# Optimization experiments

Hardware: AMD Instinct MI355X
Metric: run time of the kernel (lower is better)

The kernel has to match this reference:

```python
import jax, jax.numpy as jnp
import numpy as np

N, E, D, HID, HEADS, G = 20000, 320000, 1280, 64, 4, 256
NEG_SLOPE = 0.2  # PyG GATv2Conv default negative_slope


def setup_inputs() -> dict:
    key = jax.random.key(0)
    ks = jax.random.split(key, 20)

    def w(k, shape, fan_in):
        return (jax.random.normal(k, shape, jnp.float32) / np.float32(np.sqrt(fan_in)))

    return {
        "x": jax.random.normal(ks[0], (N, D), jnp.float32),
        "edge_index": jax.random.randint(ks[1], (2, E), 0, N),
        "batch": jnp.sort(jax.random.randint(ks[2], (N,), 0, G)),
        # GATv2 layer 1: in D, out HID, heads HEADS, concat
        "Wl1": w(ks[3], (D, HEADS * HID), D),
        "bl1": w(ks[4], (HEADS * HID,), D),
        "Wr1": w(ks[5], (D, HEADS * HID), D),
        "br1": w(ks[6], (HEADS * HID,), D),
        "att1": w(ks[7], (HEADS, HID), HID),
        "bias1": jnp.zeros((HEADS * HID,), jnp.float32),
        # GATv2 layer 2: in HEADS*HID, out HID, heads 1, concat
        "Wl2": w(ks[8], (HEADS * HID, HID), HEADS * HID),
        "bl2": w(ks[9], (HID,), HEADS * HID),
        "Wr2": w(ks[10], (HEADS * HID, HID), HEADS * HID),
        "br2": w(ks[11], (HID,), HEADS * HID),
        "att2": w(ks[12], (1, HID), HID),
        "bias2": jnp.zeros((HID,), jnp.float32),
        # MLP head
        "W3": w(ks[13], (HID, HID), HID),
        "b3": w(ks[14], (HID,), HID),
        "W4": w(ks[15], (HID, 1), HID),
        "b4": w(ks[16], (1,), HID),
    }


def _gatv2(x, src, dst, Wl, bl, Wr, br, att, bias, n):
    """PyG GATv2Conv (concat=True, eval mode): e_ij = a^T LeakyReLU(Wl x_j + Wr x_i),
    per-destination softmax, out_i = sum_j alpha_ij * (Wl x_j)."""
    H, C = att.shape
    xl = (x @ Wl + bl).reshape(n, H, C)  # source transform
    xr = (x @ Wr + br).reshape(n, H, C)  # target transform
    e = jax.nn.leaky_relu(xl[src] + xr[dst], NEG_SLOPE)      # [E,H,C]
    logit = jnp.einsum('ehc,hc->eh', e, att)                  # [E,H]
    m = jax.ops.segment_max(logit, dst, num_segments=n)      # stable softmax per dst
    ex = jnp.exp(logit - m[dst])
    denom = jax.ops.segment_sum(ex, dst, num_segments=n)
    alpha = ex / (denom[dst] + 1e-16)                         # [E,H]
    out = jax.ops.segment_sum(xl[src] * alpha[:, :, None], dst, num_segments=n)
    return out.reshape(n, H * C) + bias


def reference(x, edge_index, batch, Wl1, bl1, Wr1, br1, att1, bias1,
              Wl2, bl2, Wr2, br2, att2, bias2, W3, b3, W4, b4):
    # add_self_loops=True (PyG default)
    loops = jnp.arange(N, dtype=edge_index.dtype)
    src = jnp.concatenate([edge_index[0], loops])
    dst = jnp.concatenate([edge_index[1], loops])
    h = jax.nn.relu(_gatv2(x, src, dst, Wl1, bl1, Wr1, br1, att1, bias1, N))
    h = jax.nn.relu(_gatv2(h, src, dst, Wl2, bl2, Wr2, br2, att2, bias2, N))
    g = jax.ops.segment_sum(h, batch, num_segments=G)  # global_add_pool -> [G,HID]
    return jax.nn.relu(g @ W3 + b3) @ W4 + b4          # [G,1]
```

## Files before the change

kernel.cpp:

```cpp
#include <hip/hip_runtime.h>

constexpr int Nn    = 20000;
constexpr int Ee    = 320000;
constexpr int Dd    = 1280;
constexpr int Gg    = 256;
constexpr int ETOT  = Ee + Nn;
#define NEG 0.2f

typedef __attribute__((ext_vector_type(8))) short s8v;
typedef __attribute__((ext_vector_type(8))) unsigned short u16x8;
typedef __attribute__((ext_vector_type(4))) float f4v;

__device__ inline float lrelu(float v){ return v > 0.f ? v : NEG * v; }
__device__ inline float wave_sum(float v){
  #pragma unroll
  for(int o = 32; o; o >>= 1) v += __shfl_xor(v, o, 64);
  return v;
}
__device__ inline unsigned short f2bf(float x){
  unsigned u = __float_as_uint(x);
  return (unsigned short)((u + 0x7FFFu + ((u >> 16) & 1u)) >> 16);
}
__device__ inline float bf2f(unsigned short h){ return __uint_as_float(((unsigned)h) << 16); }

__device__ inline void async_cp16(const void* g, void* l){
  __builtin_amdgcn_global_load_lds((const __attribute__((address_space(1))) void*)g,
                                   (__attribute__((address_space(3))) void*)l, 16, 0, 0);
}

__device__ inline size_t pkoff(int n, int k, int NITp){
  return ((((size_t)(n >> 7) * NITp + (k >> 5)) * 512)
          + (((k >> 3) & 3) * 128 + (n & 127))) * 8 + (k & 7);
}

__global__ void fill_int(int* p, int n, int v){
  int i = blockIdx.x * blockDim.x + threadIdx.x;
  if(i < n) p[i] = v;
}
__global__ void hist_dst(const int* __restrict__ dst, int* __restrict__ deg){
  int e = blockIdx.x * blockDim.x + threadIdx.x;
  if(e < Ee) atomicAdd(&deg[dst[e]], 1);
}
__global__ __launch_bounds__(1024) void scan_deg(const int* __restrict__ deg,
                                                 int* __restrict__ rowptr,
                                                 int* __restrict__ cursor){
  __shared__ int part[1024];
  int t = threadIdx.x;
  const int CH = (Nn + 1023) / 1024;
  int base = t * CH;
  int s = 0;
  for(int j = 0; j < CH; j++){ int idx = base + j; if(idx < Nn) s += deg[idx]; }
  part[t] = s;
  __syncthreads();
  for(int off = 1; off < 1024; off <<= 1){
    int v = (t >= off) ? part[t - off] : 0;
    __syncthreads();
    part[t] += v;
    __syncthreads();
  }
  int acc = part[t] - s;
  for(int j = 0; j < CH; j++){
    int idx = base + j;
    if(idx < Nn){ rowptr[idx] = acc; cursor[idx] = acc; acc += deg[idx]; }
  }
  if(t == 1023) rowptr[Nn] = part[1023];
}
__global__ void scatter_edges(const int* __restrict__ src, const int* __restrict__ dst,
                              int* __restrict__ cursor, int* __restrict__ srcv){
  int e = blockIdx.x * blockDim.x + threadIdx.x;
  if(e >= ETOT) return;
  int d, s;
  if(e < Ee){ d = dst[e]; s = src[e]; } else { d = e - Ee; s = d; }
  int pos = atomicAdd(&cursor[d], 1);
  srcv[pos] = s;
}

__global__ __launch_bounds__(256) void wsplit(const float* __restrict__ Wl,
                                              const float* __restrict__ Wr,
                                              int K, int Ca, int NITp,
                                              unsigned short* __restrict__ PBH,
                                              unsigned short* __restrict__ PBL){
  __shared__ float t[32][33];
  int k0 = blockIdx.x * 32, n0 = blockIdx.y * 32;
  int tx = threadIdx.x & 31, ty = threadIdx.x >> 5;
  #pragma unroll
  for(int j = 0; j < 4; j++){
    int kk = ty + j * 8;
    int n = n0 + tx;
    t[kk][tx] = (n < Ca) ? Wl[(size_t)(k0 + kk) * Ca + n]
                         : Wr[(size_t)(k0 + kk) * Ca + (n - Ca)];
  }
  __syncthreads();
  #pragma unroll
  for(int j = 0; j < 4; j++){
    int nn = ty + j * 8;
    float v = t[tx][nn];
    unsigned short hi = f2bf(v);
    unsigned short lo = f2bf(v - bf2f(hi));
    size_t o = pkoff(n0 + nn, k0 + tx, NITp);
    PBH[o] = hi;
    PBL[o] = lo;
  }
}

__global__ __launch_bounds__(512) void gemm_2t(
    const float* __restrict__ X, int K, int niter, int ntx, int nty,
    const unsigned short* __restrict__ PBH, const unsigned short* __restrict__ PBL,
    const float* __restrict__ bl, const float* __restrict__ br, int Ca,
    float* __restrict__ Ya, float* __restrict__ Yb)
{
  int xb, yb;
  if(ntx == 4){
    int id = blockIdx.x;
    int g = id >> 5, rem = id & 31;
    xb = rem >> 3; yb = g * 8 + (rem & 7);
  } else { xb = 0; yb = blockIdx.x; }
  if(yb >= nty) return;

  __shared__ unsigned short sA [2][4096];
  __shared__ unsigned short sBh[2][4096];
  __shared__ unsigned short sBl[2][4096];

  const int tid  = threadIdx.x;
  const int lane = tid & 63;
  const int w    = tid >> 6;
  const int wm   = w & 1, wn = w >> 1;
  const int bm   = yb * 128;
  const int bn   = xb * 128;

  f4v acc[4][2] = {};

  const int ar = w * 16 + (lane >> 2);
  const int aq = lane & 3;
  int gmr = bm + ar; if(gmr >= Nn) gmr = Nn - 1;
  const float* aptr = X + (size_t)gmr * K + aq * 8;
  const int awoff = (aq * 128 + ((ar + aq * 4) & 127)) * 8;

  const size_t bbase = ((size_t)xb * niter) * 4096 + tid * 8;
  const unsigned short* bhp = PBH + bbase;
  const unsigned short* blp = PBL + bbase;
  const int bldsoff = w * 512;

  async_cp16(bhp, &sBh[0][bldsoff]);
  async_cp16(blp, &sBl[0][bldsoff]);
  {
    float4 v0 = *(const float4*)(aptr);
    float4 v1 = *(const float4*)(aptr + 4);
    float fv[8] = {v0.x, v0.y, v0.z, v0.w, v1.x, v1.y, v1.z, v1.w};
    u16x8 hv;
    #pragma unroll
    for(int q = 0; q < 8; q++) hv[q] = f2bf(fv[q]);
    *(u16x8*)&sA[0][awoff] = hv;
  }

  const int mr = lane & 15;
  const int gq = lane >> 4;
  int aoff[4], boff[2];
  #pragma unroll
  for(int i = 0; i < 4; i++){
    int row = wm * 64 + i * 16 + mr;
    aoff[i] = (gq * 128 + ((row + gq * 4) & 127)) * 8;
  }
  #pragma unroll
  for(int j = 0; j < 2; j++){
    int n = wn * 32 + j * 16 + mr;
    boff[j] = (gq * 128 + n) * 8;
  }

  for(int it = 0; it < niter; it++){
    const int cur = it & 1, nxt = cur ^ 1;
    __syncthreads();
    float4 v0, v1;
    const bool more = (it + 1 < niter);
    if(more){
      async_cp16(bhp + (size_t)(it + 1) * 4096, &sBh[nxt][bldsoff]);
      async_cp16(blp + (size_t)(it + 1) * 4096, &sBl[nxt][bldsoff]);
      v0 = *(const float4*)(aptr + (it + 1) * 32);
      v1 = *(const float4*)(aptr + (it + 1) * 32 + 4);
    }
    s8v ah[4];
    #pragma unroll
    for(int i = 0; i < 4; i++) ah[i] = *(const s8v*)&sA[cur][aoff[i]];
    #pragma unroll
    for(int j = 0; j < 2; j++){
      s8v bh  = *(const s8v*)&sBh[cur][boff[j]];
      s8v bl2 = *(const s8v*)&sBl[cur][boff[j]];
      #pragma unroll
      for(int i = 0; i < 4; i++){
        acc[i][j] = __builtin_amdgcn_mfma_f32_16x16x32_bf16(ah[i], bh,  acc[i][j], 0, 0, 0);
        acc[i][j] = __builtin_amdgcn_mfma_f32_16x16x32_bf16(ah[i], bl2, acc[i][j], 0, 0, 0);
      }
    }
    if(more){
      float fv[8] = {v0.x, v0.y, v0.z, v0.w, v1.x, v1.y, v1.z, v1.w};
      u16x8 hv;
      #pragma unroll
      for(int q = 0; q < 8; q++) hv[q] = f2bf(fv[q]);
      *(u16x8*)&sA[nxt][awoff] = hv;
    }
  }

  const int quad = lane >> 4, col = lane & 15;
  #pragma unroll
  for(int j = 0; j < 2; j++){
    int gn = bn + wn * 32 + j * 16 + col;
    const float* bias = (gn < Ca) ? bl : br;
    float*       Y    = (gn < Ca) ? Ya : Yb;
    int cn = gn & (Ca - 1);
    float bv = bias[cn];
    #pragma unroll
    for(int i = 0; i < 4; i++){
      #pragma unroll
      for(int rg = 0; rg < 4; rg++){
        int gmm = bm + wm * 64 + i * 16 + quad * 4 + rg;
        if(gmm < Nn) Y[(size_t)gmm * Ca + cn] = acc[i][j][rg] + bv;
      }
    }
  }
}

__global__ __launch_bounds__(256) void gat_fused1(
    const int* __restrict__ rowptr, const int* __restrict__ srcv,
    const float* __restrict__ XL, const float* __restrict__ XR,
    const float* __restrict__ att, const float* __restrict__ bias,
    float* __restrict__ H)
{
  int node = blockIdx.x * 4 + (threadIdx.x >> 6);
  int lane = threadIdx.x & 63;
  if(node >= Nn) return;
  const float4 xr = *(const float4*)(XR + (size_t)node * 256 + lane * 4);
  const float4 a  = *(const float4*)(att + lane * 4);
  int r0 = rowptr[node], r1 = rowptr[node + 1];
  float m[4], l[4]; float4 acc[4];
  #pragma unroll
  for(int c = 0; c < 4; c++){ m[c] = -1e30f; l[c] = 0.f; acc[c] = make_float4(0,0,0,0); }
  for(int k = r0; k < r1; k += 4){
    int nv = r1 - k;
    int s[4]; float4 xl[4]; float p[4];
    #pragma unroll
    for(int c = 0; c < 4; c++){
      int kk = (c < nv) ? (k + c) : k;
      s[c] = srcv[kk];
    }
    #pragma unroll
    for(int c = 0; c < 4; c++) xl[c] = *(const float4*)(XL + (size_t)s[c] * 256 + lane * 4);
    #pragma unroll
    for(int c = 0; c < 4; c++){
      p[c] = lrelu(xl[c].x + xr.x) * a.x + lrelu(xl[c].y + xr.y) * a.y
           + lrelu(xl[c].z + xr.z) * a.z + lrelu(xl[c].w + xr.w) * a.w;
    }
    #pragma unroll
    for(int o = 8; o; o >>= 1){
      #pragma unroll
      for(int c = 0; c < 4; c++) p[c] += __shfl_xor(p[c], o, 64);
    }
    #pragma unroll
    for(int c = 0; c < 4; c++){
      if(c < nv){
        float mn = fmaxf(m[c], p[c]);
        float sc = __expf(m[c] - mn);
        float wg = __expf(p[c] - mn);
        l[c] = l[c] * sc + wg;
        acc[c].x = acc[c].x * sc + wg * xl[c].x;
        acc[c].y = acc[c].y * sc + wg * xl[c].y;
        acc[c].z = acc[c].z * sc + wg * xl[c].z;
        acc[c].w = acc[c].w * sc + wg * xl[c].w;
        m[c] = mn;
      }
    }
  }
  float M = fmaxf(fmaxf(m[0], m[1]), fmaxf(m[2], m[3]));
  float L = 0.f; float4 A4 = make_float4(0,0,0,0);
  #pragma unroll
  for(int c = 0; c < 4; c++){
    float sc = __expf(m[c] - M);
    L += l[c] * sc;
    A4.x += acc[c].x * sc; A4.y += acc[c].y * sc;
    A4.z += acc[c].z * sc; A4.w += acc[c].w * sc;
  }
  float inv = 1.f / (L + 1e-16f);
  const float4 b = *(const float4*)(bias + lane * 4);
  float4 o;
  o.x = fmaxf(A4.x * inv + b.x, 0.f);
  o.y = fmaxf(A4.y * inv + b.y, 0.f);
  o.z = fmaxf(A4.z * inv + b.z, 0.f);
  o.w = fmaxf(A4.w * inv + b.w, 0.f);
  *(float4*)(H + (size_t)node * 256 + lane * 4) = o;
}

__global__ __launch_bounds__(256) void gat_fused2(
    const int* __restrict__ rowptr, const int* __restrict__ srcv,
    const float* __restrict__ XL, const float* __restrict__ XR,
    const float* __restrict__ att, const float* __restrict__ bias,
    float* __restrict__ H)
{
  int node = blockIdx.x * 4 + (threadIdx.x >> 6);
  int lane = threadIdx.x & 63;
  if(node >= Nn) return;
  const float xr = XR[(size_t)node * 64 + lane];
  const float a = att[lane];
  int r0 = rowptr[node], r1 = rowptr[node + 1];
  float m[4], l[4], acc[4];
  #pragma unroll
  for(int c = 0; c < 4; c++){ m[c] = -1e30f; l[c] = 0.f; acc[c] = 0.f; }
  for(int k = r0; k < r1; k += 4){
    int nv = r1 - k;
    int s[4]; float xl[4]; float p[4];
    #pragma unroll
    for(int c = 0; c < 4; c++){
      int kk = (c < nv) ? (k + c) : k;
      s[c] = srcv[kk];
    }
    #pragma unroll
    for(int c = 0; c < 4; c++) xl[c] = XL[(size_t)s[c] * 64 + lane];
    #pragma unroll
    for(int c = 0; c < 4; c++) p[c] = lrelu(xl[c] + xr) * a;
    #pragma unroll
    for(int o = 32; o; o >>= 1){
      #pragma unroll
      for(int c = 0; c < 4; c++) p[c] += __shfl_xor(p[c], o, 64);
    }
    #pragma unroll
    for(int c = 0; c < 4; c++){
      if(c < nv){
        float mn = fmaxf(m[c], p[c]);
        float sc = __expf(m[c] - mn);
        float wg = __expf(p[c] - mn);
        l[c] = l[c] * sc + wg;
        acc[c] = acc[c] * sc + wg * xl[c];
        m[c] = mn;
      }
    }
  }
  float M = fmaxf(fmaxf(m[0], m[1]), fmaxf(m[2], m[3]));
  float L = 0.f, A1 = 0.f;
  #pragma unroll
  for(int c = 0; c < 4; c++){
    float sc = __expf(m[c] - M);
    L += l[c] * sc; A1 += acc[c] * sc;
  }
  float inv = 1.f / (L + 1e-16f);
  H[(size_t)node * 64 + lane] = fmaxf(A1 * inv + bias[lane], 0.f);
}

__global__ void gbounds(const int* __restrict__ batch, int* __restrict__ gs){
  int g = blockIdx.x * blockDim.x + threadIdx.x;
  if(g > Gg) return;
  int lo = 0, hi = Nn;
  while(lo < hi){ int mid = (lo + hi) >> 1; if(batch[mid] < g) lo = mid + 1; else hi = mid; }
  gs[g] = lo;
}
__global__ __launch_bounds__(64) void pool_seg(const float* __restrict__ H2,
                                               const int* __restrict__ gs,
                                               float* __restrict__ GP){
  int g = blockIdx.x, t = threadIdx.x;
  int i0 = gs[g], i1 = gs[g + 1];
  float a0 = 0.f, a1 = 0.f, a2 = 0.f, a3 = 0.f;
  int i = i0;
  for(; i + 3 < i1; i += 4){
    a0 += H2[(size_t)i * 64 + t];       a1 += H2[(size_t)(i + 1) * 64 + t];
    a2 += H2[(size_t)(i + 2) * 64 + t]; a3 += H2[(size_t)(i + 3) * 64 + t];
  }
  for(; i < i1; i++) a0 += H2[(size_t)i * 64 + t];
  GP[(size_t)g * 64 + t] = (a0 + a1) + (a2 + a3);
}
__global__ __launch_bounds__(64) void mlp_head(const float* __restrict__ GP,
                                               const float* __restrict__ W3,
                                               const float* __restrict__ b3,
                                               const float* __restrict__ W4,
                                               const float* __restrict__ b4,
                                               float* __restrict__ out){
  int g = blockIdx.x;
  int j = threadIdx.x;
  __shared__ float sh[64];
  sh[j] = GP[(size_t)g * 64 + j];
  __syncthreads();
  float t = b3[j];
  #pragma unroll
  for(int k = 0; k < 64; k++) t = fmaf(sh[k], W3[k * 64 + j], t);
  t = fmaxf(t, 0.f);
  float p = t * W4[j];
  p = wave_sum(p);
  if(j == 0) out[g] = p + b4[0];
}

extern "C" void kernel_launch(void* const* d_in, const int* in_sizes, int n_in,
                              void* d_out, int out_size, void* d_ws, size_t ws_size,
                              hipStream_t stream)
{
  const float* x     = (const float*)d_in[0];
  const int*   ei    = (const int*)d_in[1];
  const int*   batch = (const int*)d_in[2];
  const float* Wl1   = (const float*)d_in[3];
  const float* bl1   = (const float*)d_in[4];
  const float* Wr1   = (const float*)d_in[5];
  const float* br1   = (const float*)d_in[6];
  const float* att1  = (const float*)d_in[7];
  const float* bias1 = (const float*)d_in[8];
  const float* Wl2   = (const float*)d_in[9];
  const float* bl2   = (const float*)d_in[10];
  const float* Wr2   = (const float*)d_in[11];
  const float* br2   = (const float*)d_in[12];
  const float* att2  = (const float*)d_in[13];
  const float* bias2 = (const float*)d_in[14];
  const float* W3    = (const float*)d_in[15];
  const float* b3    = (const float*)d_in[16];
  const float* W4    = (const float*)d_in[17];
  const float* b4    = (const float*)d_in[18];
  float* out = (float*)d_out;

  char* ws = (char*)d_ws;
  size_t off = 0;
  auto alloc = [&](size_t bytes) -> void* {
    void* p = ws + off;
    off += (bytes + 255) & ~(size_t)255;
    return p;
  };
  float* XL1  = (float*)alloc((size_t)Nn * 256 * 4);
  float* XR1  = (float*)alloc((size_t)Nn * 256 * 4);
  float* H1   = (float*)alloc((size_t)Nn * 256 * 4);
  unsigned short* PB1H = (unsigned short*)alloc((size_t)512 * Dd * 2);
  unsigned short* PB1L = (unsigned short*)alloc((size_t)512 * Dd * 2);
  unsigned short* PB2H = (unsigned short*)alloc((size_t)128 * 256 * 2);
  unsigned short* PB2L = (unsigned short*)alloc((size_t)128 * 256 * 2);
  int*   rowptr = (int*)alloc((size_t)(Nn + 1) * 4);
  int*   deg    = (int*)alloc((size_t)Nn * 4);
  int*   cursor = (int*)alloc((size_t)Nn * 4);
  int*   srcv   = (int*)alloc((size_t)ETOT * 4);
  float* H2   = (float*)alloc((size_t)Nn * 64 * 4);
  float* GP   = (float*)alloc((size_t)Gg * 64 * 4);
  int*   gs   = (int*)alloc((size_t)(Gg + 1) * 4);
  float* XL2 = XL1;
  float* XR2 = XR1;

  const int* srcA = ei;
  const int* dstA = ei + Ee;

  fill_int<<<(Nn + 255) / 256, 256, 0, stream>>>(deg, Nn, 1);
  hist_dst<<<(Ee + 255) / 256, 256, 0, stream>>>(dstA, deg);
  scan_deg<<<1, 1024, 0, stream>>>(deg, rowptr, cursor);
  scatter_edges<<<(ETOT + 255) / 256, 256, 0, stream>>>(srcA, dstA, cursor, srcv);
  gbounds<<<1, 512, 0, stream>>>(batch, gs);

  wsplit<<<dim3(Dd / 32, 512 / 32), 256, 0, stream>>>(Wl1, Wr1, Dd, 256, Dd / 32, PB1H, PB1L);
  wsplit<<<dim3(256 / 32, 128 / 32), 256, 0, stream>>>(Wl2, Wr2, 256, 64, 256 / 32, PB2H, PB2L);

  gemm_2t<<<640, 512, 0, stream>>>(
      x, Dd, Dd / 32, 4, (Nn + 127) / 128, PB1H, PB1L, bl1, br1, 256, XL1, XR1);
  gat_fused1<<<(Nn + 3) / 4, 256, 0, stream>>>(rowptr, srcv, XL1, XR1, att1, bias1, H1);

  gemm_2t<<<(Nn + 127) / 128, 512, 0, stream>>>(
      H1, 256, 256 / 32, 1, (Nn + 127) / 128, PB2H, PB2L, bl2, br2, 64, XL2, XR2);
  gat_fused2<<<(Nn + 3) / 4, 256, 0, stream>>>(rowptr, srcv, XL2, XR2, att2, bias2, H2);

  pool_seg<<<Gg, 64, 0, stream>>>(H2, gs, GP);
  mlp_head<<<Gg, 64, 0, stream>>>(GP, W3, b3, W4, b4, out);
}
```

Measured before the change: 466.1 us.

## Store gathered XL in bf16, prepack layer-2 activations, fuse pool and MLP

The first GEMM now writes the source-side transform XL as bf16 instead of fp32, which halves the bytes gathered per edge in both GAT aggregation kernels. gat_fused1 writes its output straight into a bf16 MFMA-packed layout. A new dedicated layer-2 GEMM loads that layout with async copies, replacing the generic conversion path. Pool and MLP head are merged into one kernel to drop a launch and an intermediate buffer. Rounding the gathered features to bf16 changes numerics slightly and adds a new packed-layout kernel.

```diff
diff --git a/kernel.cpp b/kernel.cpp
--- a/kernel.cpp
+++ b/kernel.cpp
@@ -104,17 +104,14 @@
 }
 
 __global__ __launch_bounds__(512) void gemm_2t(
-    const float* __restrict__ X, int K, int niter, int ntx, int nty,
+    const float* __restrict__ X, int K, int niter, int nty,
     const unsigned short* __restrict__ PBH, const unsigned short* __restrict__ PBL,
-    const float* __restrict__ bl, const float* __restrict__ br, int Ca,
-    float* __restrict__ Ya, float* __restrict__ Yb)
+    const float* __restrict__ bl, const float* __restrict__ br,
+    unsigned short* __restrict__ XLb, float* __restrict__ XR)
 {
-  int xb, yb;
-  if(ntx == 4){
-    int id = blockIdx.x;
-    int g = id >> 5, rem = id & 31;
-    xb = rem >> 3; yb = g * 8 + (rem & 7);
-  } else { xb = 0; yb = blockIdx.x; }
+  int id = blockIdx.x;
+  int g8 = id >> 5, rem = id & 31;
+  int xb = rem >> 3, yb = g8 * 8 + (rem & 7);
   if(yb >= nty) return;
 
   __shared__ unsigned short sA [2][4096];
@@ -204,16 +201,96 @@
   #pragma unroll
   for(int j = 0; j < 2; j++){
     int gn = bn + wn * 32 + j * 16 + col;
-    const float* bias = (gn < Ca) ? bl : br;
-    float*       Y    = (gn < Ca) ? Ya : Yb;
-    int cn = gn & (Ca - 1);
-    float bv = bias[cn];
     #pragma unroll
     for(int i = 0; i < 4; i++){
       #pragma unroll
       for(int rg = 0; rg < 4; rg++){
         int gmm = bm + wm * 64 + i * 16 + quad * 4 + rg;
-        if(gmm < Nn) Y[(size_t)gmm * Ca + cn] = acc[i][j][rg] + bv;
+        if(gmm < Nn){
+          float v = acc[i][j][rg];
+          if(gn < 256) XLb[(size_t)gmm * 256 + gn] = f2bf(v + bl[gn]);
+          else         XR [(size_t)gmm * 256 + (gn - 256)] = v + br[gn - 256];
+        }
+      }
+    }
+  }
+}
+
+__global__ __launch_bounds__(512) void gemm2_cp(
+    const unsigned short* __restrict__ PA,
+    const unsigned short* __restrict__ PBH, const unsigned short* __restrict__ PBL,
+    const float* __restrict__ bl, const float* __restrict__ br,
+    unsigned short* __restrict__ XLb, float* __restrict__ XR)
+{
+  const int yb = blockIdx.x;
+  __shared__ unsigned short sA [2][2048];
+  __shared__ unsigned short sBh[2][4096];
+  __shared__ unsigned short sBl[2][4096];
+
+  const int tid  = threadIdx.x;
+  const int lane = tid & 63;
+  const int w    = tid >> 6;
+  const int wm   = w & 1, wn = w >> 1;
+  const int bm   = yb * 64;
+  const int NIT  = 8;
+
+  f4v acc[2][2] = {};
+
+  const unsigned short* bhp = PBH + tid * 8;
+  const unsigned short* blp = PBL + tid * 8;
+  const int bldsoff = w * 512;
+  const unsigned short* pap = PA + ((size_t)yb * NIT * 256 + tid) * 8;
+  const int aldsoff = w * 512;
+
+  async_cp16(bhp, &sBh[0][bldsoff]);
+  async_cp16(blp, &sBl[0][bldsoff]);
+  if(w < 4) async_cp16(pap, &sA[0][aldsoff]);
+
+  const int mr = lane & 15;
+  const int gq = lane >> 4;
+  int aoff[2], boff[2];
+  #pragma unroll
+  for(int i = 0; i < 2; i++) aoff[i] = (gq * 64 + wm * 32 + i * 16 + mr) * 8;
+  #pragma unroll
+  for(int j = 0; j < 2; j++) boff[j] = (gq * 128 + wn * 32 + j * 16 + mr) * 8;
+
+  for(int it = 0; it < NIT; it++){
+    const int cur = it & 1, nxt = cur ^ 1;
+    __syncthreads();
+    if(it + 1 < NIT){
+      async_cp16(bhp + (size_t)(it + 1) * 4096, &sBh[nxt][bldsoff]);
+      async_cp16(blp + (size_t)(it + 1) * 4096, &sBl[nxt][bldsoff]);
+      if(w < 4) async_cp16(pap + (size_t)(it + 1) * 2048, &sA[nxt][aldsoff]);
+    }
+    s8v ah[2];
+    #pragma unroll
+    for(int i = 0; i < 2; i++) ah[i] = *(const s8v*)&sA[cur][aoff[i]];
+    #pragma unroll
+    for(int j = 0; j < 2; j++){
+      s8v bh  = *(const s8v*)&sBh[cur][boff[j]];
+      s8v bl2 = *(const s8v*)&sBl[cur][boff[j]];
+      #pragma unroll
+      for(int i = 0; i < 2; i++){
+        acc[i][j] = __builtin_amdgcn_mfma_f32_16x16x32_bf16(ah[i], bh,  acc[i][j], 0, 0, 0);
+        acc[i][j] = __builtin_amdgcn_mfma_f32_16x16x32_bf16(ah[i], bl2, acc[i][j], 0, 0, 0);
+      }
+    }
+  }
+
+  const int quad = lane >> 4, col = lane & 15;
+  #pragma unroll
+  for(int j = 0; j < 2; j++){
+    int gn = wn * 32 + j * 16 + col;
+    #pragma unroll
+    for(int i = 0; i < 2; i++){
+      #pragma unroll
+      for(int rg = 0; rg < 4; rg++){
+        int gmm = bm + wm * 32 + i * 16 + quad * 4 + rg;
+        if(gmm < Nn){
+          float v = acc[i][j][rg];
+          if(gn < 64) XLb[(size_t)gmm * 64 + gn] = f2bf(v + bl[gn]);
+          else        XR [(size_t)gmm * 64 + (gn - 64)] = v + br[gn - 64];
+        }
       }
     }
   }
@@ -221,9 +298,9 @@
 
 __global__ __launch_bounds__(256) void gat_fused1(
     const int* __restrict__ rowptr, const int* __restrict__ srcv,
-    const float* __restrict__ XL, const float* __restrict__ XR,
+    const unsigned short* __restrict__ XLb, const float* __restrict__ XR,
     const float* __restrict__ att, const float* __restrict__ bias,
-    float* __restrict__ H)
+    unsigned short* __restrict__ PA2)
 {
   int node = blockIdx.x * 4 + (threadIdx.x >> 6);
   int lane = threadIdx.x & 63;
@@ -243,7 +320,10 @@
       s[c] = srcv[kk];
     }
     #pragma unroll
-    for(int c = 0; c < 4; c++) xl[c] = *(const float4*)(XL + (size_t)s[c] * 256 + lane * 4);
+    for(int c = 0; c < 4; c++){
+      ushort4 u = *(const ushort4*)(XLb + (size_t)s[c] * 256 + lane * 4);
+      xl[c] = make_float4(bf2f(u.x), bf2f(u.y), bf2f(u.z), bf2f(u.w));
+    }
     #pragma unroll
     for(int c = 0; c < 4; c++){
       p[c] = lrelu(xl[c].x + xr.x) * a.x + lrelu(xl[c].y + xr.y) * a.y
@@ -285,12 +365,14 @@
   o.y = fmaxf(A4.y * inv + b.y, 0.f);
   o.z = fmaxf(A4.z * inv + b.z, 0.f);
   o.w = fmaxf(A4.w * inv + b.w, 0.f);
-  *(float4*)(H + (size_t)node * 256 + lane * 4) = o;
+  size_t po = ((((size_t)(node >> 6) * 8 + (lane >> 3)) * 256)
+               + ((lane >> 1) & 3) * 64 + (node & 63)) * 8 + (lane & 1) * 4;
+  *(ushort4*)(PA2 + po) = make_ushort4(f2bf(o.x), f2bf(o.y), f2bf(o.z), f2bf(o.w));
 }
 
 __global__ __launch_bounds__(256) void gat_fused2(
     const int* __restrict__ rowptr, const int* __restrict__ srcv,
-    const float* __restrict__ XL, const float* __restrict__ XR,
+    const unsigned short* __restrict__ XLb, const float* __restrict__ XR,
     const float* __restrict__ att, const float* __restrict__ bias,
     float* __restrict__ H)
 {
@@ -312,7 +394,7 @@
       s[c] = srcv[kk];
     }
     #pragma unroll
-    for(int c = 0; c < 4; c++) xl[c] = XL[(size_t)s[c] * 64 + lane];
+    for(int c = 0; c < 4; c++) xl[c] = bf2f(XLb[(size_t)s[c] * 64 + lane]);
     #pragma unroll
     for(int c = 0; c < 4; c++) p[c] = lrelu(xl[c] + xr) * a;
     #pragma unroll
@@ -350,9 +432,13 @@
   while(lo < hi){ int mid = (lo + hi) >> 1; if(batch[mid] < g) lo = mid + 1; else hi = mid; }
   gs[g] = lo;
 }
-__global__ __launch_bounds__(64) void pool_seg(const float* __restrict__ H2,
+__global__ __launch_bounds__(64) void pool_mlp(const float* __restrict__ H2,
                                                const int* __restrict__ gs,
-                                               float* __restrict__ GP){
+                                               const float* __restrict__ W3,
+                                               const float* __restrict__ b3,
+                                               const float* __restrict__ W4,
+                                               const float* __restrict__ b4,
+                                               float* __restrict__ out){
   int g = blockIdx.x, t = threadIdx.x;
   int i0 = gs[g], i1 = gs[g + 1];
   float a0 = 0.f, a1 = 0.f, a2 = 0.f, a3 = 0.f;
@@ -362,26 +448,16 @@
     a2 += H2[(size_t)(i + 2) * 64 + t]; a3 += H2[(size_t)(i + 3) * 64 + t];
   }
   for(; i < i1; i++) a0 += H2[(size_t)i * 64 + t];
-  GP[(size_t)g * 64 + t] = (a0 + a1) + (a2 + a3);
-}
-__global__ __launch_bounds__(64) void mlp_head(const float* __restrict__ GP,
-                                               const float* __restrict__ W3,
-                                               const float* __restrict__ b3,
-                                               const float* __restrict__ W4,
-                                               const float* __restrict__ b4,
-                                               float* __restrict__ out){
-  int g = blockIdx.x;
-  int j = threadIdx.x;
   __shared__ float sh[64];
-  sh[j] = GP[(size_t)g * 64 + j];
+  sh[t] = (a0 + a1) + (a2 + a3);
   __syncthreads();
-  float t = b3[j];
-  #pragma unroll
-  for(int k = 0; k < 64; k++) t = fmaf(sh[k], W3[k * 64 + j], t);
-  t = fmaxf(t, 0.f);
-  float p = t * W4[j];
+  float acc = b3[t];
+  #pragma unroll
+  for(int k = 0; k < 64; k++) acc = fmaf(sh[k], W3[k * 64 + t], acc);
+  acc = fmaxf(acc, 0.f);
+  float p = acc * W4[t];
   p = wave_sum(p);
-  if(j == 0) out[g] = p + b4[0];
+  if(t == 0) out[g] = p + b4[0];
 }
 
 extern "C" void kernel_launch(void* const* d_in, const int* in_sizes, int n_in,
@@ -416,9 +492,13 @@
     off += (bytes + 255) & ~(size_t)255;
     return p;
   };
-  float* XL1  = (float*)alloc((size_t)Nn * 256 * 4);
-  float* XR1  = (float*)alloc((size_t)Nn * 256 * 4);
-  float* H1   = (float*)alloc((size_t)Nn * 256 * 4);
+  const int NTY1 = (Nn + 127) / 128;
+  const int NTY2 = (Nn + 63) / 64;
+  unsigned short* XLb1 = (unsigned short*)alloc((size_t)Nn * 256 * 2);
+  float*          XR1  = (float*)alloc((size_t)Nn * 256 * 4);
+  unsigned short* PA2  = (unsigned short*)alloc((size_t)NTY2 * 8 * 256 * 8 * 2);
+  unsigned short* XLb2 = (unsigned short*)alloc((size_t)Nn * 64 * 2);
+  float*          XR2  = (float*)alloc((size_t)Nn * 64 * 4);
   unsigned short* PB1H = (unsigned short*)alloc((size_t)512 * Dd * 2);
   unsigned short* PB1L = (unsigned short*)alloc((size_t)512 * Dd * 2);
   unsigned short* PB2H = (unsigned short*)alloc((size_t)128 * 256 * 2);
@@ -428,10 +508,7 @@
   int*   cursor = (int*)alloc((size_t)Nn * 4);
   int*   srcv   = (int*)alloc((size_t)ETOT * 4);
   float* H2   = (float*)alloc((size_t)Nn * 64 * 4);
-  float* GP   = (float*)alloc((size_t)Gg * 64 * 4);
   int*   gs   = (int*)alloc((size_t)(Gg + 1) * 4);
-  float* XL2 = XL1;
-  float* XR2 = XR1;
 
   const int* srcA = ei;
   const int* dstA = ei + Ee;
@@ -446,13 +523,11 @@
   wsplit<<<dim3(256 / 32, 128 / 32), 256, 0, stream>>>(Wl2, Wr2, 256, 64, 256 / 32, PB2H, PB2L);
 
   gemm_2t<<<640, 512, 0, stream>>>(
-      x, Dd, Dd / 32, 4, (Nn + 127) / 128, PB1H, PB1L, bl1, br1, 256, XL1, XR1);
-  gat_fused1<<<(Nn + 3) / 4, 256, 0, stream>>>(rowptr, srcv, XL1, XR1, att1, bias1, H1);
-
-  gemm_2t<<<(Nn + 127) / 128, 512, 0, stream>>>(
-      H1, 256, 256 / 32, 1, (Nn + 127) / 128, PB2H, PB2L, bl2, br2, 64, XL2, XR2);
-  gat_fused2<<<(Nn + 3) / 4, 256, 0, stream>>>(rowptr, srcv, XL2, XR2, att2, bias2, H2);
-
-  pool_seg<<<Gg, 64, 0, stream>>>(H2, gs, GP);
-  mlp_head<<<Gg, 64, 0, stream>>>(GP, W3, b3, W4, b4, out);
-}
+      x, Dd, Dd / 32, NTY1, PB1H, PB1L, bl1, br1, XLb1, XR1);
+  gat_fused1<<<(Nn + 3) / 4, 256, 0, stream>>>(rowptr, srcv, XLb1, XR1, att1, bias1, PA2);
+
+  gemm2_cp<<<NTY2, 512, 0, stream>>>(PA2, PB2H, PB2L, bl2, br2, XLb2, XR2);
+  gat_fused2<<<(Nn + 3) / 4, 256, 0, stream>>>(rowptr, srcv, XLb2, XR2, att2, bias2, H2);
+
+  pool_mlp<<<Gg, 64, 0, stream>>>(H2, gs, W3, b3, W4, b4, out);
+}
```

Result: faster. 452.9 us (-2.8%).
